# Optimization experiments

Hardware: AMD Instinct MI355X
Metric: run time of the kernel (lower is better)

## Reference

```python
import jax, jax.numpy as jnp
import numpy as np

B, N, D, H = 8, 4096, 256, 4
KP, KN = N // 16, N // 32
EPS = 1e-6

def _ln(x, g, b):
    m = jnp.mean(x, -1, keepdims=True)
    v = jnp.var(x, -1, keepdims=True)
    return (x - m) / jnp.sqrt(v + 1e-5) * g + b

def _cross_attn(q_in, kv_in, wq, wk, wv, wo, bo):
    # q_in [1,Nq,D], kv_in [1,Nk,D]
    Bq, Nq, Dm = q_in.shape
    Nk = kv_in.shape[1]
    dh = Dm // H
    q = (q_in @ wq).reshape(Bq, Nq, H, dh).transpose(0, 2, 1, 3)
    k = (kv_in @ wk).reshape(Bq, Nk, H, dh).transpose(0, 2, 1, 3)
    v = (kv_in @ wv).reshape(Bq, Nk, H, dh).transpose(0, 2, 1, 3)
    attn = jax.nn.softmax(jnp.einsum('bhqd,bhkd->bhqk', q, k) * (dh ** -0.5), axis=-1)
    out = jnp.einsum('bhqk,bhkd->bhqd', attn, v).transpose(0, 2, 1, 3).reshape(Bq, Nq, Dm)
    return out @ wo + bo

def setup_inputs():
    key = jax.random.key(0)
    ks = jax.random.split(key, 40)
    f32 = jnp.float32
    def w(i, shape, s):
        return s * jax.random.normal(ks[i], shape, f32)
    inp = {}
    inp['x'] = jax.random.normal(ks[0], (B, N, D), f32)
    inp['mask'] = (jax.random.randint(ks[1], (B, N), 0, 3) - 1).astype(jnp.int32)  # values in {-1,0,1}
    inp['pos_emb'] = 0.02 * jax.random.normal(ks[2], (1, N, D), f32)
    inp['sim_p_w'] = w(3, (D, D), 0.2); inp['sim_p_b'] = jnp.zeros((D,), f32)
    inp['sim_n_w'] = w(4, (D, D), 0.2); inp['sim_n_b'] = jnp.zeros((D,), f32)
    inp['adj_w'] = w(5, (D, D), 0.05)
    inp['gnn_p_w1'] = w(6, (D, D), 0.05); inp['gnn_p_w2'] = w(7, (D, D), 0.05)
    inp['gnn_n_w1'] = w(8, (D, D), 0.05); inp['gnn_n_w2'] = w(9, (D, D), 0.05)
    for i in range(1, 6):
        inp['ln%d_g' % i] = jnp.ones((D,), f32)
        inp['ln%d_b' % i] = jnp.zeros((D,), f32)
    names = ['i2q_wq', 'i2q_wk', 'i2q_wv', 'i2q_wo', 'q2i_wq', 'q2i_wk', 'q2i_wv', 'q2i_wo']
    for j, nme in enumerate(names):
        inp[nme] = w(10 + j, (D, D), 0.05)
    inp['i2q_bo'] = jnp.zeros((D,), f32)
    inp['q2i_bo'] = jnp.zeros((D,), f32)
    inp['mlp_w'] = w(20, (D, D), 0.05); inp['mlp_b'] = jnp.zeros((D,), f32)
    inp['g_i2t'] = 0.1 * jax.random.normal(ks[21], (1, 1, D), f32)
    inp['g_t2i'] = 0.1 * jax.random.normal(ks[22], (1, 1, D), f32)
    return inp

def reference(x, mask, pos_emb, sim_p_w, sim_p_b, sim_n_w, sim_n_b, adj_w,
              gnn_p_w1, gnn_p_w2, gnn_n_w1, gnn_n_w2,
              ln1_g, ln1_b, ln2_g, ln2_b, ln3_g, ln3_b, ln4_g, ln4_b, ln5_g, ln5_b,
              i2q_wq, i2q_wk, i2q_wv, i2q_wo, i2q_bo,
              q2i_wq, q2i_wk, q2i_wv, q2i_wo, q2i_bo,
              mlp_w, mlp_b, g_i2t, g_t2i):
    pos_mask = (mask == 1).astype(x.dtype)[..., None]    # [B,N,1]
    neg_mask = (mask == -1).astype(x.dtype)[..., None]
    pos_query = (x * pos_mask).sum(1, keepdims=True) / (pos_mask.sum(1, keepdims=True) + EPS)  # [B,1,D]
    neg_query = (x * neg_mask).sum(1, keepdims=True) / (neg_mask.sum(1, keepdims=True) + EPS)
    pos_sim = jax.nn.sigmoid(((x @ sim_p_w + sim_p_b) * pos_query).sum(-1))  # [B,N]
    neg_sim = jax.nn.sigmoid(((x @ sim_n_w + sim_n_b) * neg_query).sum(-1))
    weight_p, idx_p = jax.lax.top_k(pos_sim, KP)
    weight_n, idx_n = jax.lax.top_k(neg_sim, KN)
    scale = 1.0 / jnp.sqrt(jnp.asarray(D, x.dtype))

    def gcn(node, w1, w2):
        adj = jax.nn.softmax((node @ adj_w) @ node.T * scale, axis=-1)  # [K,K]
        h = jax.nn.relu(adj @ (node @ w1))
        return adj @ (h @ w2)

    def batch_forward(ip, wp, inn, wn, feat):
        node_p = feat[ip] * (wp > 0.6).astype(feat.dtype)[:, None]       # [KP,D]
        query_p = gcn(node_p, gnn_p_w1, gnn_p_w2) + pos_emb[0, ip]
        node_n = feat[inn] * (wn > 0.6).astype(feat.dtype)[:, None]      # [KN,D]
        query_n = gcn(node_n, gnn_n_w1, gnn_n_w2) + pos_emb[0, inn]
        query = jnp.concatenate([query_p, query_n], 0)[None]             # [1,KP+KN,D]
        featb = feat[None]                                               # [1,N,D]
        query = query + g_i2t * _cross_attn(_ln(query, ln1_g, ln1_b), _ln(featb, ln2_g, ln2_b),
                                            i2q_wq, i2q_wk, i2q_wv, i2q_wo, i2q_bo)
        featb = featb + g_t2i * _cross_attn(_ln(featb, ln3_g, ln3_b), _ln(query, ln4_g, ln4_b),
                                            q2i_wq, q2i_wk, q2i_wv, q2i_wo, q2i_bo)
        featb = featb + (_ln(featb, ln5_g, ln5_b) @ mlp_w + mlp_b)
        return featb

    out = jax.vmap(batch_forward)(idx_p, weight_p, idx_n, weight_n, x)   # [B,1,N,D]
    return out, pos_sim, neg_sim
```

## Files before the change

### kernel.cpp

```cpp
#include <hip/hip_runtime.h>

#define BB 8
#define NN 4096
#define DD 256
#define HH 4
#define DHH 64
#define KPP 256
#define KNN 128
#define SCH 64

typedef float f32x4 __attribute__((ext_vector_type(4)));
typedef short bf16x8 __attribute__((ext_vector_type(8)));
typedef short bf16x4 __attribute__((ext_vector_type(4)));

#define FLAG_TRANSB 1
#define FLAG_RELU   2

__device__ __forceinline__ float bf2f(unsigned short u){
  union { unsigned int i; float f; } v; v.i = ((unsigned int)u) << 16; return v.f;
}
__device__ __forceinline__ unsigned short f2bf(float f){
  union { float f; unsigned int i; } v; v.f = f;
  return (unsigned short)((v.i + 0x7FFFu + ((v.i >> 16) & 1u)) >> 16);
}
__device__ __forceinline__ void gload16(const void* g, void* l){
  __builtin_amdgcn_global_load_lds((const __attribute__((address_space(1))) void*)g,
                                   (__attribute__((address_space(3))) void*)l, 16, 0, 0);
}

__global__ __launch_bounds__(256) void stats_part(const float* __restrict__ x,
                                                  const int* __restrict__ mask,
                                                  float* __restrict__ part,
                                                  float* __restrict__ pcnt){
  int b = blockIdx.y, c = blockIdx.x, t = threadIdx.x;
  int w = t >> 6, lane = t & 63;
  const int R = NN / SCH;
  int n0 = c * R;
  const float* xb = x + ((long)b*NN + n0)*DD;
  const int* mb = mask + (long)b*NN + n0;
// ... 71 lines not shown
  float s  = xv.x+xv.y+xv.z+xv.w;
  float q  = xv.x*xv.x+xv.y*xv.y+xv.z*xv.z+xv.w*xv.w;
  for (int off = 32; off; off >>= 1){
    sp += __shfl_xor(sp, off); sn += __shfl_xor(sn, off);
    s  += __shfl_xor(s, off);  q  += __shfl_xor(q, off);
  }
  float m = s*(1.f/256.f);
  float var = q*(1.f/256.f) - m*m;
  float rinv = rsqrtf(var + 1e-5f);
  ushort4 o;
  o.x = f2bf((xv.x-m)*rinv); o.y = f2bf((xv.y-m)*rinv);
  o.z = f2bf((xv.z-m)*rinv); o.w = f2bf((xv.w-m)*rinv);
  ((ushort4*)(xhat + row*DD))[lane] = o;
  if (lane == 0){
    float zp = sp + cscal[b*2+0], zn = sn + cscal[b*2+1];
    simP[row] = 1.f/(1.f+expf(-zp));
    simN[row] = 1.f/(1.f+expf(-zn));
  }
}

__global__ __launch_bounds__(256) void topk_radix(const float* __restrict__ simP,
                                                  const float* __restrict__ simN,
                                                  const float* __restrict__ x,
                                                  int* __restrict__ idxb, float* __restrict__ wb,
                                                  float* __restrict__ node){
  __shared__ unsigned int vals[4096];
  __shared__ unsigned int hist[4096];
  __shared__ unsigned short eql[4096];
  __shared__ unsigned int tsum[256];
  __shared__ unsigned int sB, sRem, sCG, sCnt, sEq;
  int id = blockIdx.x; int sgn = id & 1, b = id >> 1;
  int K = (sgn == 0) ? KPP : KNN;
  const float* s = (sgn == 0 ? simP : simN) + (long)b*NN;
  int t = threadIdx.x;
  if (t == 0){ sCG = 0; sCnt = 0; sEq = 0; }
  for (int i = t; i < 4096; i += 256){ vals[i] = __float_as_uint(s[i]); hist[i] = 0; }
  __syncthreads();

  auto find_thresh = [&](int NB, unsigned need){
    int per = NB >> 8;
    int base = t*per;
    unsigned local = 0;
    for (int j = 0; j < per; j++) local += hist[base+j];
    tsum[t] = local;
    __syncthreads();
    #pragma unroll
    for (int st = 1; st < 256; st <<= 1){
      unsigned v = (t + st < 256) ? tsum[t+st] : 0u;
// ... 29 lines not shown
    unsigned v = vals[i];
    if ((v >> 20) == B1) atomicAdd(&hist[(v >> 8) & 0xFFFu], 1u);
  }
  __syncthreads();
  find_thresh(4096, rem1);
  unsigned B2 = sB, rem2 = sRem;
  unsigned pre = (B1 << 12) | B2;
  __syncthreads();
  hist[t] = 0;
  __syncthreads();
  for (int i = t; i < 4096; i += 256){
    unsigned v = vals[i];
    if ((v >> 8) == pre) atomicAdd(&hist[v & 0xFFu], 1u);
  }
  __syncthreads();
  find_thresh(256, rem2);
  unsigned T = (pre << 8) | sB;
  unsigned cg = sCG;
  __syncthreads();
  hist[t] = 0;
  __syncthreads();

  int* oi = idxb + (long)id*256;
  float* ow = wb + (long)id*256;
  for (int i = t; i < 4096; i += 256){
    unsigned v = vals[i];
    if (v > T){
      unsigned p = atomicAdd(&sCnt, 1u);
      oi[p] = i; ow[p] = __uint_as_float(v);
      hist[p] = (unsigned)i; hist[256+p] = v;
    }
    else if (v == T){ unsigned e = atomicAdd(&sEq, 1u); eql[e] = (unsigned short)i; }
  }
  __syncthreads();
  int ne = K - (int)cg;
  int eqn = (int)sEq;
  for (int e = t; e < eqn; e += 256){
    int myi = eql[e]; int r = 0;
    for (int e2 = 0; e2 < eqn; e2++) r += (eql[e2] < myi);
    if (r < ne){
      oi[cg + r] = myi; ow[cg + r] = __uint_as_float(T);
      hist[cg + r] = (unsigned)myi; hist[256 + cg + r] = T;
    }
  }
  __syncthreads();
  int rbase = (sgn == 0) ? 0 : KPP;
  int lane = t & 63, rw = t >> 6;
  for (int i0 = 0; i0 < K; i0 += 4){
    int r = i0 + rw;
    int idx = (int)hist[r];
    float wv = __uint_as_float(hist[256 + r]);
    float4 vsel;
    if (wv > 0.6f) vsel = ((const float4*)(x + ((long)b*NN + idx)*DD))[lane];
    else vsel = (float4){0.f,0.f,0.f,0.f};
    ((float4*)(node + ((long)b*384 + rbase + r)*DD))[lane] = vsel;
  }
}

__global__ void softmax_dual(float* __restrict__ A0, int L0, int rpb0, long bs0, int rows0,
                             float* __restrict__ A1, int L1, int rpb1, long bs1, int rows1){
  int w = threadIdx.x >> 6, lane = threadIdx.x & 63;
  long row = (long)blockIdx.x*4 + w;
  float* A; int L, rpb; long bs;
  if (row < rows0){ A = A0; L = L0; rpb = rpb0; bs = bs0; }
  else { row -= rows0; if (row >= rows1) return; A = A1; L = L1; rpb = rpb1; bs = bs1; }
  int b = (int)(row / rpb), r = (int)(row % rpb);
  float* a = A + (long)b*bs + (long)r*L;
  int e = L >> 6;
  float vals[4]; float mx = -1e30f;
  for (int j = 0; j < e; j++){ vals[j] = a[lane*e+j]; mx = fmaxf(mx, vals[j]); }
  for (int off = 32; off; off >>= 1) mx = fmaxf(mx, __shfl_xor(mx, off));
  float sum = 0.f;
  for (int j = 0; j < e; j++){ vals[j] = expf(vals[j]-mx); sum += vals[j]; }
  for (int off = 32; off; off >>= 1) sum += __shfl_xor(sum, off);
  float rinv = 1.f/sum;
  for (int j = 0; j < e; j++) a[lane*e+j] = vals[j]*rinv;
}

__global__ void rownorm_kernel(const float* __restrict__ X, unsigned short* __restrict__ Y, int rows){
  int w = threadIdx.x >> 6, lane = threadIdx.x & 63;
  long row = (long)blockIdx.x*4 + w;
  if (row >= rows) return;
  const float4* xr = (const float4*)(X + row*DD);
  float4 xv = xr[lane];
  float s = xv.x+xv.y+xv.z+xv.w;
  float q = xv.x*xv.x+xv.y*xv.y+xv.z*xv.z+xv.w*xv.w;
  for (int off = 32; off; off >>= 1){ s += __shfl_xor(s, off); q += __shfl_xor(q, off); }
  float m = s*(1.f/256.f);
  float var = q*(1.f/256.f) - m*m;
  float rinv = rsqrtf(var + 1e-5f);
  ushort4 o;
  o.x = f2bf((xv.x-m)*rinv); o.y = f2bf((xv.y-m)*rinv);
  o.z = f2bf((xv.z-m)*rinv); o.w = f2bf((xv.w-m)*rinv);
  ((ushort4*)(Y + row*DD))[lane] = o;
}

struct FoldArgs { const float* W[9]; const float* g[9]; unsigned short* BT[9]; };
struct BiasArgs { const float* W[7]; const float* b[7]; const float* addb[7]; float* out[7]; };

__global__ void fold_w(FoldArgs fa){
  int m = blockIdx.y, tile = blockIdx.x, t = threadIdx.x;
  const float* W = fa.W[m]; const float* g = fa.g[m]; unsigned short* BT = fa.BT[m];
  __shared__ float T[64][65];
  int tn = (tile & 3)*64, tk = (tile >> 2)*64;
  #pragma unroll 4
  for (int p = 0; p < 16; p++){
    int kl = p*4 + (t >> 6), nl = t & 63;
    float v = W[(long)(tk+kl)*256 + tn + nl];
    if (g) v *= g[tk+kl];
    T[kl][nl] = v;
  }
  __syncthreads();
  #pragma unroll 4
  for (int p = 0; p < 16; p++){
    int nl = p*4 + (t >> 6), kl = t & 63;
    BT[(long)(tn+nl)*256 + tk + kl] = f2bf(T[kl][nl]);
  }
}

__global__ void fold_b(BiasArgs ba){
  int m = blockIdx.x, n = threadIdx.x;
  const float* W = ba.W[m]; const float* b = ba.b[m];
  float s = (ba.addb[m] != nullptr) ? ba.addb[m][n] : 0.f;
  for (int k = 0; k < 256; k++) s += b[k]*W[(long)k*256+n];
  ba.out[m][n] = s;
}

struct GP {
  const float* A; long sAb; int lda;
  const float* B; long sBb; int ldb;
  float* C; long sCb; int ldc;
  const int* pidx; const float* pe;
  int M, N, K; float alpha; int flags;
};
struct GP4 { GP p[4]; };

__global__ __launch_bounds__(256) void gemm_multi(GP4 g4){
  GP p = g4.p[blockIdx.z >> 3];
  int b = blockIdx.z & 7;
  int m0 = blockIdx.y*64, n0 = blockIdx.x*64;
  if (m0 >= p.M || n0 >= p.N) return;
  __shared__ __align__(16) unsigned short As[64*40];
  __shared__ __align__(16) unsigned short Bs[64*40];
  const float* Ab = p.A + (long)b*p.sAb;
  const float* Bb = p.B + (long)b*p.sBb;
  int t = threadIdx.x;
  int w = t >> 6, lane = t & 63, lrowi = lane & 15, lquad = lane >> 4;
  int wm = w >> 1, wn = w & 1;
  f32x4 acc[2][2];
  #pragma unroll
  for (int i = 0; i < 2; i++)
    #pragma unroll
    for (int j = 0; j < 2; j++) acc[i][j] = (f32x4){0.f,0.f,0.f,0.f};
  int am = t >> 2, akq = t & 3;
  for (int k0 = 0; k0 < p.K; k0 += 32){
    {
      const float4* s4 = (const float4*)(Ab + (long)(m0+am)*p.lda + k0 + akq*8);
      float4 u = s4[0], vv = s4[1];
      unsigned short tmp[8];
      tmp[0]=f2bf(u.x); tmp[1]=f2bf(u.y); tmp[2]=f2bf(u.z); tmp[3]=f2bf(u.w);
      tmp[4]=f2bf(vv.x); tmp[5]=f2bf(vv.y); tmp[6]=f2bf(vv.z); tmp[7]=f2bf(vv.w);
      *(uint4*)(&As[am*40 + akq*8]) = *(uint4*)tmp;
    }
    if (p.flags & FLAG_TRANSB){
      const float4* s4 = (const float4*)(Bb + (long)(n0+am)*p.ldb + k0 + akq*8);
      float4 u = s4[0], vv = s4[1];
      unsigned short tmp[8];
      tmp[0]=f2bf(u.x); tmp[1]=f2bf(u.y); tmp[2]=f2bf(u.z); tmp[3]=f2bf(u.w);
      tmp[4]=f2bf(vv.x); tmp[5]=f2bf(vv.y); tmp[6]=f2bf(vv.z); tmp[7]=f2bf(vv.w);
      *(uint4*)(&Bs[am*40 + akq*8]) = *(uint4*)tmp;
    } else {
      int bn = t & 63, bkb = (t >> 6)*8;
      #pragma unroll
      for (int j = 0; j < 8; j++)
        Bs[bn*40 + bkb + j] = f2bf(Bb[(long)(k0+bkb+j)*p.ldb + n0 + bn]);
    }
    __syncthreads();
    bf16x8 af[2], bfr[2];
    #pragma unroll
    for (int i = 0; i < 2; i++)
      af[i] = *(const bf16x8*)(&As[(wm*32 + i*16 + lrowi)*40 + lquad*8]);
    #pragma unroll
    for (int j = 0; j < 2; j++)
      bfr[j] = *(const bf16x8*)(&Bs[(wn*32 + j*16 + lrowi)*40 + lquad*8]);
    #pragma unroll
    for (int i = 0; i < 2; i++)
      #pragma unroll
      for (int j = 0; j < 2; j++)
        acc[i][j] = __builtin_amdgcn_mfma_f32_16x16x32_bf16(af[i], bfr[j], acc[i][j], 0, 0, 0);
    __syncthreads();
  }
  float* Cb = p.C + (long)b*p.sCb;
  #pragma unroll
  for (int i = 0; i < 2; i++)
    #pragma unroll
    for (int j = 0; j < 2; j++){
      int col = n0 + wn*32 + j*16 + lrowi;
      #pragma unroll
      for (int r = 0; r < 4; r++){
        int row = m0 + wm*32 + i*16 + lquad*4 + r;
        float v = p.alpha*acc[i][j][r];
        if (p.flags & FLAG_RELU) v = fmaxf(v, 0.f);
        if (p.pidx != nullptr){
          int idx = p.pidx[b*512 + row];
          v += p.pe[(long)idx*256 + col];
        }
        Cb[(long)row*p.ldc + col] = v;
      }
    }
}

template<typename OT, bool RES, bool GATE>
__global__ __launch_bounds__(256) void gemm128(
    const unsigned short* __restrict__ A, long sAb,
    const unsigned short* __restrict__ BT,
    OT* __restrict__ C, long sCb, int ldc,
    const float* __restrict__ R, long sRb,
    const float* __restrict__ bias, const float* __restrict__ gate)
{
  __shared__ __align__(16) unsigned short As[4096];
  __shared__ __align__(16) unsigned short Bs[4096];
  int t = threadIdx.x;
  int w = t >> 6, lane = t & 63, lrowi = lane & 15, lquad = lane >> 4;
  int wm = w >> 1, wn = w & 1;
  int m0 = blockIdx.y*128, n0 = blockIdx.x*128;
  const unsigned short* Ab = A + (long)blockIdx.z*sAb + (long)m0*256;
  const unsigned short* Bb = BT + (long)n0*256;
  int g0 = t, g1 = 256 + t;
  int row0 = g0 >> 2, kq0 = g0 & 3;
  int row1 = g1 >> 2, kq1 = g1 & 3;
  f32x4 acc[4][4];
  #pragma unroll
// ... 32 lines not shown
    for (int i = 0; i < 4; i++){
      #pragma unroll
      for (int r = 0; r < 4; r++){
        int row = m0 + wm*64 + i*16 + lquad*4 + r;
        float v = acc[i][j][r] + bv;
        if (GATE) v *= gv;
        if (RES) v += Rb[(long)row*256 + col];
        if constexpr (sizeof(OT) == 4) Cb[(long)row*ldc + col] = v;
        else                           Cb[(long)row*ldc + col] = f2bf(v);
      }
    }
  }
}

template<int NFRAG>
__global__ __launch_bounds__(256) void flash_kernel(
    const unsigned short* __restrict__ Q, long sQb, int ldq,
    const unsigned short* __restrict__ Kt, const unsigned short* __restrict__ Vt,
    long sKb, int ldkv,
    unsigned short* __restrict__ O, long sOb,
    float* __restrict__ Opart, float* __restrict__ Lpart,
    int Nq, int Nk, int nsplit, float scale)
{
  __shared__ __align__(16) unsigned short Kl[32*72];
  __shared__ __align__(16) unsigned short Vl[64*36];
  __shared__ __align__(16) unsigned short Pl[4*NFRAG*16*36];
  int b = blockIdx.z, h = blockIdx.y;
  int nqg = Nq / (64*NFRAG);
  int qg = blockIdx.x % nqg, split = blockIdx.x / nqg;
  int kchunk = Nk / nsplit;
  int kbeg = split*kchunk, kend = kbeg + kchunk;
  int t = threadIdx.x, w = t >> 6, lane = t & 63, lrowi = lane & 15, lquad = lane >> 4;
  int q0 = qg*(64*NFRAG) + w*(16*NFRAG);
  const unsigned short* Qb = Q + (long)b*sQb + h*DHH;
  const unsigned short* Kb = Kt + (long)b*sKb + h*DHH;
  const unsigned short* Vb = Vt + (long)b*sKb + h*DHH;
  bf16x8 qa[NFRAG][2];
  #pragma unroll
  for (int f = 0; f < NFRAG; f++)
    #pragma unroll
    for (int kt = 0; kt < 2; kt++)
      qa[f][kt] = *(const bf16x8*)(Qb + (long)(q0 + f*16 + lrowi)*ldq + kt*32 + lquad*8);

  f32x4 o[NFRAG][4];
  float psum[NFRAG][4];
  #pragma unroll
  for (int f = 0; f < NFRAG; f++)
    #pragma unroll
    for (int cj = 0; cj < 4; cj++){
      o[f][cj] = (f32x4){0.f,0.f,0.f,0.f};
      psum[f][cj] = 0.f;
    }
  int skq = t >> 3, sdq = (t & 7)*8;
  int vkq = t & 31, vdq = (t >> 5)*8;
  unsigned short* Pw = &Pl[w*(NFRAG*16*36)];
  const float ec = scale * 1.44269504089f;

  for (int kt0 = kbeg; kt0 < kend; kt0 += 32){
    {
      uint4 kv = *(const uint4*)(Kb + (long)(kt0+skq)*ldkv + sdq);
      *(uint4*)(&Kl[skq*72 + sdq]) = kv;
      uint4 vv = *(const uint4*)(Vb + (long)(kt0+vkq)*ldkv + vdq);
      const unsigned short* vp = (const unsigned short*)&vv;
      #pragma unroll
      for (int j = 0; j < 8; j++) Vl[(vdq+j)*36 + vkq] = vp[j];
    }
    __syncthreads();
    bf16x8 kb0 = *(const bf16x8*)(&Kl[(0*16+lrowi)*72 + lquad*8]);
    bf16x8 kb1 = *(const bf16x8*)(&Kl[(0*16+lrowi)*72 + 32 + lquad*8]);
    bf16x8 kb2 = *(const bf16x8*)(&Kl[(1*16+lrowi)*72 + lquad*8]);
    bf16x8 kb3 = *(const bf16x8*)(&Kl[(1*16+lrowi)*72 + 32 + lquad*8]);
    union { bf16x8 v8; bf16x4 v4[2]; } vbu[4];
    #pragma unroll
    for (int cj = 0; cj < 4; cj++){
      const unsigned short* vb = &Vl[(cj*16+lrowi)*36 + lquad*8];
      vbu[cj].v4[0] = *(const bf16x4*)vb;
      vbu[cj].v4[1] = *(const bf16x4*)(vb + 4);
    }
    #pragma unroll
    for (int f = 0; f < NFRAG; f++){
      f32x4 S0 = (f32x4){0.f,0.f,0.f,0.f}, S1 = (f32x4){0.f,0.f,0.f,0.f};
      S0 = __builtin_amdgcn_mfma_f32_16x16x32_bf16(qa[f][0], kb0, S0, 0, 0, 0);
      S0 = __builtin_amdgcn_mfma_f32_16x16x32_bf16(qa[f][1], kb1, S0, 0, 0, 0);
      S1 = __builtin_amdgcn_mfma_f32_16x16x32_bf16(qa[f][0], kb2, S1, 0, 0, 0);
      S1 = __builtin_amdgcn_mfma_f32_16x16x32_bf16(qa[f][1], kb3, S1, 0, 0, 0);
      unsigned short* Pf = Pw + f*(16*36);
      #pragma unroll
      for (int r = 0; r < 4; r++){
        float p0 = exp2f(S0[r]*ec);
        float p1 = exp2f(S1[r]*ec);
        psum[f][r] += p0 + p1;
        Pf[(lquad*4+r)*36 + lrowi]      = f2bf(p0);
        Pf[(lquad*4+r)*36 + 16 + lrowi] = f2bf(p1);
      }
    }
    __asm__ volatile("s_waitcnt lgkmcnt(0)" ::: "memory");
    #pragma unroll
    for (int f = 0; f < NFRAG; f++){
      const unsigned short* pp = &Pw[f*(16*36) + lrowi*36 + lquad*8];
      union { bf16x8 v8; bf16x4 v4[2]; } pa;
      pa.v4[0] = *(const bf16x4*)pp;
      pa.v4[1] = *(const bf16x4*)(pp + 4);
      #pragma unroll
      for (int cj = 0; cj < 4; cj++)
        o[f][cj] = __builtin_amdgcn_mfma_f32_16x16x32_bf16(pa.v8, vbu[cj].v8, o[f][cj], 0, 0, 0);
    }
    __syncthreads();
  }
  float lsum[NFRAG][4];
  #pragma unroll
  for (int f = 0; f < NFRAG; f++)
    #pragma unroll
    for (int r = 0; r < 4; r++){
      float s = psum[f][r];
      #pragma unroll
      for (int off = 1; off < 16; off <<= 1) s += __shfl_xor(s, off);
      lsum[f][r] = s;
    }
  if (nsplit > 1){
    int p = (b*HH + h)*nsplit + split;
    float* Op = Opart + (long)p*Nq*DHH;
    #pragma unroll
    for (int f = 0; f < NFRAG; f++)
      #pragma unroll
      for (int r = 0; r < 4; r++){
        int row = q0 + f*16 + lquad*4 + r;
        #pragma unroll
        for (int cj = 0; cj < 4; cj++)
// ... 62 lines not shown
  const float* i2q_bo = (const float*)d_in[30];
  const float* q2i_bo = (const float*)d_in[31];
  const float* mlp_w  = (const float*)d_in[32];
  const float* mlp_b  = (const float*)d_in[33];
  const float* g_i2t  = (const float*)d_in[34];
  const float* g_t2i  = (const float*)d_in[35];

  float* out  = (float*)d_out;
  float* simP = out + (size_t)BB*NN*DD;
  float* simN = simP + (size_t)BB*NN;

  char* w8 = (char*)d_ws;
  size_t off = 0;
  auto take = [&](size_t bytes)->void*{
    void* p = (void*)(w8 + off);
    off += (bytes + 255) & ~(size_t)255;
    return p;
  };
  float* part   = (float*)take((size_t)BB*SCH*2*DD*4);
  float* pcnt   = (float*)take((size_t)BB*SCH*2*4);
  float* vvec   = (float*)take((size_t)BB*2*DD*4);
  float* cscal  = (float*)take((size_t)BB*2*4);
  int*   idxb   = (int*)take((size_t)BB*2*256*4);
  float* wb     = (float*)take((size_t)BB*2*256*4);
  float* node   = (float*)take((size_t)BB*384*DD*4);
  float* gA     = (float*)take((size_t)BB*384*DD*4);
  float* gadjP  = (float*)take((size_t)BB*256*256*4);
  float* gadjN  = (float*)take((size_t)BB*128*128*4);
  float* query  = (float*)take((size_t)BB*384*DD*4);
  float* query2 = (float*)take((size_t)BB*384*DD*4);
  unsigned short* xhatq  = (unsigned short*)take((size_t)BB*384*DD*2);
  unsigned short* qh     = (unsigned short*)take((size_t)BB*384*DD*2);
  unsigned short* attnZ  = (unsigned short*)take((size_t)BB*384*DD*2);
  unsigned short* xhatq2 = (unsigned short*)take((size_t)BB*384*DD*2);
  unsigned short* kv2    = (unsigned short*)take((size_t)BB*384*512*2);
  unsigned short* xhat   = (unsigned short*)take((size_t)BB*NN*DD*2);
  unsigned short* kvq    = (unsigned short*)take((size_t)BB*NN*768*2);
  float* featb2 = (float*)take((size_t)BB*NN*DD*4);
  float* Lpart  = (float*)take((size_t)BB*HH*8*384*4);
  unsigned short* wTq1  = (unsigned short*)take((size_t)65536*2);
  unsigned short* wTbig = (unsigned short*)take((size_t)3*65536*2);
  unsigned short* wTkv2 = (unsigned short*)take((size_t)2*65536*2);
  unsigned short* wTmlp = (unsigned short*)take((size_t)65536*2);
  unsigned short* wTo1  = (unsigned short*)take((size_t)65536*2);
  unsigned short* wTo2  = (unsigned short*)take((size_t)65536*2);
  float* biasQ1  = (float*)take(256*4);
  float* biasBig = (float*)take(768*4);
  float* biasKV2 = (float*)take(512*4);
  float* biasMlp = (float*)take(256*4);
  float* t1 = query;
  float* t2 = query2;
  float* t3 = gA;
  unsigned short* attn2 = xhat;
  unsigned short* xhat5 = kvq;
  float* Opart = featb2;

  const long sQ  = 384L*DD;
  const long sX  = (long)NN*DD;
  const float* NF = nullptr;

  FoldArgs fa;
  fa.W[0]=i2q_wq; fa.g[0]=ln1_g; fa.BT[0]=wTq1;
  fa.W[1]=i2q_wk; fa.g[1]=ln2_g; fa.BT[1]=wTbig;
  fa.W[2]=i2q_wv; fa.g[2]=ln2_g; fa.BT[2]=wTbig + 256*256;
  fa.W[3]=q2i_wq; fa.g[3]=ln3_g; fa.BT[3]=wTbig + 512*256;
  fa.W[4]=q2i_wk; fa.g[4]=ln4_g; fa.BT[4]=wTkv2;
  fa.W[5]=q2i_wv; fa.g[5]=ln4_g; fa.BT[5]=wTkv2 + 256*256;
  fa.W[6]=mlp_w;  fa.g[6]=ln5_g; fa.BT[6]=wTmlp;
  fa.W[7]=i2q_wo; fa.g[7]=nullptr; fa.BT[7]=wTo1;
  fa.W[8]=q2i_wo; fa.g[8]=nullptr; fa.BT[8]=wTo2;
  fold_w<<<dim3(16,9), 256, 0, stream>>>(fa);
  BiasArgs ba;
  ba.W[0]=i2q_wq; ba.b[0]=ln1_b; ba.addb[0]=nullptr; ba.out[0]=biasQ1;
  ba.W[1]=i2q_wk; ba.b[1]=ln2_b; ba.addb[1]=nullptr; ba.out[1]=biasBig;
  ba.W[2]=i2q_wv; ba.b[2]=ln2_b; ba.addb[2]=nullptr; ba.out[2]=biasBig+256;
  ba.W[3]=q2i_wq; ba.b[3]=ln3_b; ba.addb[3]=nullptr; ba.out[3]=biasBig+512;
  ba.W[4]=q2i_wk; ba.b[4]=ln4_b; ba.addb[4]=nullptr; ba.out[4]=biasKV2;
  ba.W[5]=q2i_wv; ba.b[5]=ln4_b; ba.addb[5]=nullptr; ba.out[5]=biasKV2+256;
  ba.W[6]=mlp_w;  ba.b[6]=ln5_b; ba.addb[6]=mlp_b;   ba.out[6]=biasMlp;
  fold_b<<<7, 256, 0, stream>>>(ba);

  stats_part<<<dim3(SCH, BB), 256, 0, stream>>>(x, mask, part, pcnt);
  stats_vec<<<BB, 256, 0, stream>>>(part, pcnt, sim_p_w, sim_p_b, sim_n_w, sim_n_b, vvec, cscal);
  sim_norm_kernel<<<dim3(NN/4, BB), 256, 0, stream>>>(x, vvec, cscal, simP, simN, xhat);
  topk_radix<<<2*BB, 256, 0, stream>>>(simP, simN, x, idxb, wb, node);

  GP z = {};
  {
    GP4 g;
    g.p[0] = { node, 384L*DD, 256, adj_w, 0, 256, gA, 384L*DD, 256, nullptr, nullptr, 384, 256, 256, 1.f, 0 };
    g.p[1] = { node, 384L*DD, 256, gnn_p_w1, 0, 256, t1, 384L*DD, 256, nullptr, nullptr, 256, 256, 256, 1.f, 0 };
    g.p[2] = { node + 256L*DD, 384L*DD, 256, gnn_n_w1, 0, 256, t1 + 256L*DD, 384L*DD, 256, nullptr, nullptr, 128, 256, 256, 1.f, 0 };
    g.p[3] = z;
    gemm_multi<<<dim3(4,6,3*BB), 256, 0, stream>>>(g);
  }
  {
    GP4 g;
    g.p[0] = { gA, 384L*DD, 256, node, 384L*DD, 256, gadjP, 65536L, 256, nullptr, nullptr, 256, 256, 256, 0.0625f, FLAG_TRANSB };
    g.p[1] = { gA + 256L*DD, 384L*DD, 256, node + 256L*DD, 384L*DD, 256, gadjN, 16384L, 128, nullptr, nullptr, 128, 128, 256, 0.0625f, FLAG_TRANSB };
    g.p[2] = z; g.p[3] = z;
    gemm_multi<<<dim3(4,4,2*BB), 256, 0, stream>>>(g);
  }
  softmax_dual<<<768, 256, 0, stream>>>(gadjP, 256, 256, 65536L, BB*256,
                                        gadjN, 128, 128, 16384L, BB*128);
  {
    GP4 g;
    g.p[0] = { gadjP, 65536L, 256, t1, 384L*DD, 256, t2, 384L*DD, 256, nullptr, nullptr, 256, 256, 256, 1.f, FLAG_RELU };
    g.p[1] = { gadjN, 16384L, 128, t1 + 256L*DD, 384L*DD, 256, t2 + 256L*DD, 384L*DD, 256, nullptr, nullptr, 128, 256, 128, 1.f, FLAG_RELU };
    g.p[2] = z; g.p[3] = z;
    gemm_multi<<<dim3(4,4,2*BB), 256, 0, stream>>>(g);
  }
  {
    GP4 g;
    g.p[0] = { t2, 384L*DD, 256, gnn_p_w2, 0, 256, t3, 384L*DD, 256, nullptr, nullptr, 256, 256, 256, 1.f, 0 };
    g.p[1] = { t2 + 256L*DD, 384L*DD, 256, gnn_n_w2, 0, 256, t3 + 256L*DD, 384L*DD, 256, nullptr, nullptr, 128, 256, 256, 1.f, 0 };
    g.p[2] = z; g.p[3] = z;
    gemm_multi<<<dim3(4,4,2*BB), 256, 0, stream>>>(g);
  }
  {
    GP4 g;
    g.p[0] = { gadjP, 65536L, 256, t3, 384L*DD, 256, query, 384L*DD, 256, idxb, pos_emb, 256, 256, 256, 1.f, 0 };
    g.p[1] = { gadjN, 16384L, 128, t3 + 256L*DD, 384L*DD, 256, query + 256L*DD, 384L*DD, 256, idxb + 256, pos_emb, 128, 256, 128, 1.f, 0 };
    g.p[2] = z; g.p[3] = z;
    gemm_multi<<<dim3(4,4,2*BB), 256, 0, stream>>>(g);
  }

  rownorm_kernel<<<BB*384/4, 256, 0, stream>>>(query, xhatq, BB*384);

  gemm128<unsigned short,false,false><<<dim3(2,3,BB),256,0,stream>>>(
      xhatq, sQ, wTq1, qh, sQ, 256, NF, 0, biasQ1, NF);
  gemm128<unsigned short,false,false><<<dim3(6,32,BB),256,0,stream>>>(
      xhat, sX, wTbig, kvq, (long)NN*768, 768, NF, 0, biasBig, NF);
  flash_kernel<3><<<dim3(2*8, HH, BB), 256, 0, stream>>>(
      qh, sQ, 256, kvq, kvq + 256, (long)NN*768, 768,
      attnZ, sQ, Opart, Lpart, 384, NN, 8, 0.125f);
  flash_combine<<<BB*HH*384/4, 256, 0, stream>>>(Opart, Lpart, attnZ, sQ, 384, 8);
  gemm128<float,true,true><<<dim3(2,3,BB),256,0,stream>>>(
      attnZ, sQ, wTo1, query2, sQ, 256, query, sQ, i2q_bo, g_i2t);

  rownorm_kernel<<<BB*384/4, 256, 0, stream>>>(query2, xhatq2, BB*384);
  gemm128<unsigned short,false,false><<<dim3(4,3,BB),256,0,stream>>>(
      xhatq2, sQ, wTkv2, kv2, 384L*512, 512, NF, 0, biasKV2, NF);
  flash_kernel<2><<<dim3(32, HH, BB), 256, 0, stream>>>(
      kvq + 512, (long)NN*768, 768, kv2, kv2 + 256, 384L*512, 512,
      attn2, sX, nullptr, nullptr, NN, 384, 1, 0.125f);
  gemm128<float,true,true><<<dim3(2,32,BB),256,0,stream>>>(
      attn2, sX, wTo2, featb2, sX, 256, x, sX, q2i_bo, g_t2i);
// ... 6 lines not shown
```

Baseline: 498.6 us.

## Convert GCN chain to bf16 NT GEMMs with async LDS loads; widen flash K tile

The GCN stage now keeps node features, adjacency, and intermediate products in bf16. Weights are pre-transposed in fold_w, and each product is arranged so both operands are K-contiguous. This lets a new 128x128 GEMM load tiles straight into LDS with global_load_lds instead of converting fp32 on the fly, and it removes the strided transpose-B path. Separately, the flash attention inner loop now processes 64 keys per iteration with packed V transposes and truncating bf16 conversion of P. The cost is extra bf16 buffers, more rounding in intermediate GCN results, and larger LDS and register use per block.

```diff
diff --git a/kernel.cpp b/kernel.cpp
--- a/kernel.cpp
+++ b/kernel.cpp
@@ -11,10 +11,9 @@
 
 typedef float f32x4 __attribute__((ext_vector_type(4)));
 typedef short bf16x8 __attribute__((ext_vector_type(8)));
-typedef short bf16x4 __attribute__((ext_vector_type(4)));
-
-#define FLAG_TRANSB 1
-#define FLAG_RELU   2
+
+#define FLAG_RELU   1
+#define FLAG_OUTF32 2
 
 __device__ __forceinline__ float bf2f(unsigned short u){
   union { unsigned int i; float f; } v; v.i = ((unsigned int)u) << 16; return v.f;
@@ -132,8 +131,8 @@
 __global__ __launch_bounds__(256) void topk_radix(const float* __restrict__ simP,
                                                   const float* __restrict__ simN,
                                                   const float* __restrict__ x,
-                                                  int* __restrict__ idxb, float* __restrict__ wb,
-                                                  float* __restrict__ node){
+                                                  int* __restrict__ idxb,
+                                                  unsigned short* __restrict__ node_bf){
   __shared__ unsigned int vals[4096];
   __shared__ unsigned int hist[4096];
   __shared__ unsigned short eql[4096];
@@ -209,12 +208,11 @@
   __syncthreads();
 
   int* oi = idxb + (long)id*256;
-  float* ow = wb + (long)id*256;
   for (int i = t; i < 4096; i += 256){
     unsigned v = vals[i];
     if (v > T){
       unsigned p = atomicAdd(&sCnt, 1u);
-      oi[p] = i; ow[p] = __uint_as_float(v);
+      oi[p] = i;
       hist[p] = (unsigned)i; hist[256+p] = v;
     }
     else if (v == T){ unsigned e = atomicAdd(&sEq, 1u); eql[e] = (unsigned short)i; }
@@ -226,7 +224,7 @@
     int myi = eql[e]; int r = 0;
     for (int e2 = 0; e2 < eqn; e2++) r += (eql[e2] < myi);
     if (r < ne){
-      oi[cg + r] = myi; ow[cg + r] = __uint_as_float(T);
+      oi[cg + r] = myi;
       hist[cg + r] = (unsigned)myi; hist[256 + cg + r] = T;
     }
   }
@@ -240,19 +238,24 @@
     float4 vsel;
     if (wv > 0.6f) vsel = ((const float4*)(x + ((long)b*NN + idx)*DD))[lane];
     else vsel = (float4){0.f,0.f,0.f,0.f};
-    ((float4*)(node + ((long)b*384 + rbase + r)*DD))[lane] = vsel;
-  }
-}
-
-__global__ void softmax_dual(float* __restrict__ A0, int L0, int rpb0, long bs0, int rows0,
-                             float* __restrict__ A1, int L1, int rpb1, long bs1, int rows1){
+    ushort4 ov;
+    ov.x = f2bf(vsel.x); ov.y = f2bf(vsel.y); ov.z = f2bf(vsel.z); ov.w = f2bf(vsel.w);
+    ((ushort4*)(node_bf + ((long)b*384 + rbase + r)*DD))[lane] = ov;
+  }
+}
+
+__global__ void softmax_dual(const float* __restrict__ A0, unsigned short* __restrict__ O0,
+                             int L0, int rpb0, long bs0, int rows0,
+                             const float* __restrict__ A1, unsigned short* __restrict__ O1,
+                             int L1, int rpb1, long bs1, int rows1){
   int w = threadIdx.x >> 6, lane = threadIdx.x & 63;
   long row = (long)blockIdx.x*4 + w;
-  float* A; int L, rpb; long bs;
-  if (row < rows0){ A = A0; L = L0; rpb = rpb0; bs = bs0; }
-  else { row -= rows0; if (row >= rows1) return; A = A1; L = L1; rpb = rpb1; bs = bs1; }
+  const float* A; unsigned short* O; int L, rpb; long bs;
+  if (row < rows0){ A = A0; O = O0; L = L0; rpb = rpb0; bs = bs0; }
+  else { row -= rows0; if (row >= rows1) return; A = A1; O = O1; L = L1; rpb = rpb1; bs = bs1; }
   int b = (int)(row / rpb), r = (int)(row % rpb);
-  float* a = A + (long)b*bs + (long)r*L;
+  const float* a = A + (long)b*bs + (long)r*L;
+  unsigned short* o = O + (long)b*bs + (long)r*L;
   int e = L >> 6;
   float vals[4]; float mx = -1e30f;
   for (int j = 0; j < e; j++){ vals[j] = a[lane*e+j]; mx = fmaxf(mx, vals[j]); }
@@ -261,7 +264,7 @@
   for (int j = 0; j < e; j++){ vals[j] = expf(vals[j]-mx); sum += vals[j]; }
   for (int off = 32; off; off >>= 1) sum += __shfl_xor(sum, off);
   float rinv = 1.f/sum;
-  for (int j = 0; j < e; j++) a[lane*e+j] = vals[j]*rinv;
+  for (int j = 0; j < e; j++) o[lane*e+j] = f2bf(vals[j]*rinv);
 }
 
 __global__ void rownorm_kernel(const float* __restrict__ X, unsigned short* __restrict__ Y, int rows){
@@ -282,7 +285,7 @@
   ((ushort4*)(Y + row*DD))[lane] = o;
 }
 
-struct FoldArgs { const float* W[9]; const float* g[9]; unsigned short* BT[9]; };
+struct FoldArgs { const float* W[14]; const float* g[14]; unsigned short* BT[14]; };
 struct BiasArgs { const float* W[7]; const float* b[7]; const float* addb[7]; float* out[7]; };
 
 __global__ void fold_w(FoldArgs fa){
@@ -313,88 +316,78 @@
   ba.out[m][n] = s;
 }
 
-struct GP {
-  const float* A; long sAb; int lda;
-  const float* B; long sBb; int ldb;
-  float* C; long sCb; int ldc;
+struct GX {
+  const unsigned short* A; long sAb; int lda;
+  const unsigned short* B; long sBb; int ldb;
+  void* C; long sCb; int ldc;
   const int* pidx; const float* pe;
   int M, N, K; float alpha; int flags;
 };
-struct GP4 { GP p[4]; };
-
-__global__ __launch_bounds__(256) void gemm_multi(GP4 g4){
-  GP p = g4.p[blockIdx.z >> 3];
+struct GX4 { GX p[4]; };
+
+__global__ __launch_bounds__(256) void gemmx(GX4 g4){
+  GX p = g4.p[blockIdx.z >> 3];
   int b = blockIdx.z & 7;
-  int m0 = blockIdx.y*64, n0 = blockIdx.x*64;
+  int m0 = blockIdx.y*128, n0 = blockIdx.x*128;
   if (m0 >= p.M || n0 >= p.N) return;
-  __shared__ __align__(16) unsigned short As[64*40];
-  __shared__ __align__(16) unsigned short Bs[64*40];
-  const float* Ab = p.A + (long)b*p.sAb;
-  const float* Bb = p.B + (long)b*p.sBb;
+  __shared__ __align__(16) unsigned short As[4096];
+  __shared__ __align__(16) unsigned short Bs[4096];
   int t = threadIdx.x;
   int w = t >> 6, lane = t & 63, lrowi = lane & 15, lquad = lane >> 4;
   int wm = w >> 1, wn = w & 1;
-  f32x4 acc[2][2];
+  const unsigned short* Ab = p.A + (long)b*p.sAb + (long)m0*p.lda;
+  const unsigned short* Bb = p.B + (long)b*p.sBb + (long)n0*p.ldb;
+  int g0 = t, g1 = 256 + t;
+  int row0 = g0 >> 2, kq0 = g0 & 3;
+  int row1 = g1 >> 2, kq1 = g1 & 3;
+  f32x4 acc[4][4];
   #pragma unroll
-  for (int i = 0; i < 2; i++)
-    #pragma unroll
-    for (int j = 0; j < 2; j++) acc[i][j] = (f32x4){0.f,0.f,0.f,0.f};
-  int am = t >> 2, akq = t & 3;
+  for (int i = 0; i < 4; i++)
+    #pragma unroll
+    for (int j = 0; j < 4; j++) acc[i][j] = (f32x4){0.f,0.f,0.f,0.f};
+
   for (int k0 = 0; k0 < p.K; k0 += 32){
-    {
-      const float4* s4 = (const float4*)(Ab + (long)(m0+am)*p.lda + k0 + akq*8);
-      float4 u = s4[0], vv = s4[1];
-      unsigned short tmp[8];
-      tmp[0]=f2bf(u.x); tmp[1]=f2bf(u.y); tmp[2]=f2bf(u.z); tmp[3]=f2bf(u.w);
-      tmp[4]=f2bf(vv.x); tmp[5]=f2bf(vv.y); tmp[6]=f2bf(vv.z); tmp[7]=f2bf(vv.w);
-      *(uint4*)(&As[am*40 + akq*8]) = *(uint4*)tmp;
-    }
-    if (p.flags & FLAG_TRANSB){
-      const float4* s4 = (const float4*)(Bb + (long)(n0+am)*p.ldb + k0 + akq*8);
-      float4 u = s4[0], vv = s4[1];
-      unsigned short tmp[8];
-      tmp[0]=f2bf(u.x); tmp[1]=f2bf(u.y); tmp[2]=f2bf(u.z); tmp[3]=f2bf(u.w);
-      tmp[4]=f2bf(vv.x); tmp[5]=f2bf(vv.y); tmp[6]=f2bf(vv.z); tmp[7]=f2bf(vv.w);
-      *(uint4*)(&Bs[am*40 + akq*8]) = *(uint4*)tmp;
-    } else {
-      int bn = t & 63, bkb = (t >> 6)*8;
-      #pragma unroll
-      for (int j = 0; j < 8; j++)
-        Bs[bn*40 + bkb + j] = f2bf(Bb[(long)(k0+bkb+j)*p.ldb + n0 + bn]);
-    }
+    gload16(Ab + (long)row0*p.lda + k0 + kq0*8, &As[g0*8]);
+    gload16(Ab + (long)row1*p.lda + k0 + kq1*8, &As[g1*8]);
+    gload16(Bb + (long)row0*p.ldb + k0 + kq0*8, &Bs[g0*8]);
+    gload16(Bb + (long)row1*p.ldb + k0 + kq1*8, &Bs[g1*8]);
     __syncthreads();
-    bf16x8 af[2], bfr[2];
-    #pragma unroll
-    for (int i = 0; i < 2; i++)
-      af[i] = *(const bf16x8*)(&As[(wm*32 + i*16 + lrowi)*40 + lquad*8]);
-    #pragma unroll
-    for (int j = 0; j < 2; j++)
-      bfr[j] = *(const bf16x8*)(&Bs[(wn*32 + j*16 + lrowi)*40 + lquad*8]);
-    #pragma unroll
-    for (int i = 0; i < 2; i++)
-      #pragma unroll
-      for (int j = 0; j < 2; j++)
+    bf16x8 af[4], bfr[4];
+    #pragma unroll
+    for (int i = 0; i < 4; i++)
+      af[i] = *(const bf16x8*)(&As[((wm*64 + i*16 + lrowi)*4 + lquad)*8]);
+    #pragma unroll
+    for (int j = 0; j < 4; j++)
+      bfr[j] = *(const bf16x8*)(&Bs[((wn*64 + j*16 + lrowi)*4 + lquad)*8]);
+    #pragma unroll
+    for (int i = 0; i < 4; i++)
+      #pragma unroll
+      for (int j = 0; j < 4; j++)
         acc[i][j] = __builtin_amdgcn_mfma_f32_16x16x32_bf16(af[i], bfr[j], acc[i][j], 0, 0, 0);
     __syncthreads();
   }
-  float* Cb = p.C + (long)b*p.sCb;
+  char* Cb = (char*)p.C;
   #pragma unroll
-  for (int i = 0; i < 2; i++)
-    #pragma unroll
-    for (int j = 0; j < 2; j++){
-      int col = n0 + wn*32 + j*16 + lrowi;
+  for (int j = 0; j < 4; j++){
+    int col = n0 + wn*64 + j*16 + lrowi;
+    #pragma unroll
+    for (int i = 0; i < 4; i++){
       #pragma unroll
       for (int r = 0; r < 4; r++){
-        int row = m0 + wm*32 + i*16 + lquad*4 + r;
+        int row = m0 + wm*64 + i*16 + lquad*4 + r;
         float v = p.alpha*acc[i][j][r];
         if (p.flags & FLAG_RELU) v = fmaxf(v, 0.f);
         if (p.pidx != nullptr){
           int idx = p.pidx[b*512 + row];
           v += p.pe[(long)idx*256 + col];
         }
-        Cb[(long)row*p.ldc + col] = v;
+        if (p.flags & FLAG_OUTF32)
+          ((float*)Cb)[b*p.sCb + (long)row*p.ldc + col] = v;
+        else
+          ((unsigned short*)Cb)[b*p.sCb + (long)row*p.ldc + col] = f2bf(v);
       }
     }
+  }
 }
 
 template<typename OT, bool RES, bool GATE>
@@ -473,9 +466,9 @@
     float* __restrict__ Opart, float* __restrict__ Lpart,
     int Nq, int Nk, int nsplit, float scale)
 {
-  __shared__ __align__(16) unsigned short Kl[32*72];
-  __shared__ __align__(16) unsigned short Vl[64*36];
-  __shared__ __align__(16) unsigned short Pl[4*NFRAG*16*36];
+  __shared__ __align__(16) unsigned short Kl[64*72];
+  __shared__ __align__(16) unsigned short Vl[64*72];
+  __shared__ __align__(16) unsigned short Pl[4*NFRAG*16*72];
   int b = blockIdx.z, h = blockIdx.y;
   int nqg = Nq / (64*NFRAG);
   int qg = blockIdx.x % nqg, split = blockIdx.x / nqg;
@@ -503,58 +496,68 @@
       psum[f][cj] = 0.f;
     }
   int skq = t >> 3, sdq = (t & 7)*8;
-  int vkq = t & 31, vdq = (t >> 5)*8;
-  unsigned short* Pw = &Pl[w*(NFRAG*16*36)];
+  int vkp = t & 31, vdg = t >> 5;
+  unsigned short* Pw = &Pl[w*(NFRAG*16*72)];
   const float ec = scale * 1.44269504089f;
 
-  for (int kt0 = kbeg; kt0 < kend; kt0 += 32){
+  for (int kt0 = kbeg; kt0 < kend; kt0 += 64){
     {
-      uint4 kv = *(const uint4*)(Kb + (long)(kt0+skq)*ldkv + sdq);
-      *(uint4*)(&Kl[skq*72 + sdq]) = kv;
-      uint4 vv = *(const uint4*)(Vb + (long)(kt0+vkq)*ldkv + vdq);
-      const unsigned short* vp = (const unsigned short*)&vv;
-      #pragma unroll
-      for (int j = 0; j < 8; j++) Vl[(vdq+j)*36 + vkq] = vp[j];
+      uint4 k0v = *(const uint4*)(Kb + (long)(kt0+skq)*ldkv + sdq);
+      *(uint4*)(&Kl[skq*72 + sdq]) = k0v;
+      uint4 k1v = *(const uint4*)(Kb + (long)(kt0+32+skq)*ldkv + sdq);
+      *(uint4*)(&Kl[(32+skq)*72 + sdq]) = k1v;
+      uint4 v0 = *(const uint4*)(Vb + (long)(kt0+2*vkp)*ldkv + vdg*8);
+      uint4 v1 = *(const uint4*)(Vb + (long)(kt0+2*vkp+1)*ldkv + vdg*8);
+      const unsigned short* p0 = (const unsigned short*)&v0;
+      const unsigned short* p1 = (const unsigned short*)&v1;
+      #pragma unroll
+      for (int j = 0; j < 8; j++){
+        unsigned pk = (unsigned)p0[j] | ((unsigned)p1[j] << 16);
+        *(unsigned*)(&Vl[(vdg*8+j)*72 + 2*vkp]) = pk;
+      }
     }
     __syncthreads();
-    bf16x8 kb0 = *(const bf16x8*)(&Kl[(0*16+lrowi)*72 + lquad*8]);
-    bf16x8 kb1 = *(const bf16x8*)(&Kl[(0*16+lrowi)*72 + 32 + lquad*8]);
-    bf16x8 kb2 = *(const bf16x8*)(&Kl[(1*16+lrowi)*72 + lquad*8]);
-    bf16x8 kb3 = *(const bf16x8*)(&Kl[(1*16+lrowi)*72 + 32 + lquad*8]);
-    union { bf16x8 v8; bf16x4 v4[2]; } vbu[4];
+    bf16x8 kbf[4][2];
+    #pragma unroll
+    for (int ct = 0; ct < 4; ct++){
+      kbf[ct][0] = *(const bf16x8*)(&Kl[(ct*16+lrowi)*72 + lquad*8]);
+      kbf[ct][1] = *(const bf16x8*)(&Kl[(ct*16+lrowi)*72 + 32 + lquad*8]);
+    }
+    #pragma unroll
+    for (int f = 0; f < NFRAG; f++){
+      f32x4 S[4];
+      #pragma unroll
+      for (int ct = 0; ct < 4; ct++){
+        S[ct] = (f32x4){0.f,0.f,0.f,0.f};
+        S[ct] = __builtin_amdgcn_mfma_f32_16x16x32_bf16(qa[f][0], kbf[ct][0], S[ct], 0, 0, 0);
+        S[ct] = __builtin_amdgcn_mfma_f32_16x16x32_bf16(qa[f][1], kbf[ct][1], S[ct], 0, 0, 0);
+      }
+      unsigned short* Pf = Pw + f*(16*72);
+      #pragma unroll
+      for (int ct = 0; ct < 4; ct++)
+        #pragma unroll
+        for (int r = 0; r < 4; r++){
+          float p = exp2f(S[ct][r]*ec);
+          psum[f][r] += p;
+          Pf[(lquad*4+r)*72 + ct*16 + lrowi] = (unsigned short)(__float_as_uint(p) >> 16);
+        }
+    }
+    __asm__ volatile("s_waitcnt lgkmcnt(0)" ::: "memory");
+    bf16x8 vbf[4][2];
     #pragma unroll
     for (int cj = 0; cj < 4; cj++){
-      const unsigned short* vb = &Vl[(cj*16+lrowi)*36 + lquad*8];
-      vbu[cj].v4[0] = *(const bf16x4*)vb;
-      vbu[cj].v4[1] = *(const bf16x4*)(vb + 4);
+      vbf[cj][0] = *(const bf16x8*)(&Vl[(cj*16+lrowi)*72 + lquad*8]);
+      vbf[cj][1] = *(const bf16x8*)(&Vl[(cj*16+lrowi)*72 + 32 + lquad*8]);
     }
     #pragma unroll
     for (int f = 0; f < NFRAG; f++){
-      f32x4 S0 = (f32x4){0.f,0.f,0.f,0.f}, S1 = (f32x4){0.f,0.f,0.f,0.f};
-      S0 = __builtin_amdgcn_mfma_f32_16x16x32_bf16(qa[f][0], kb0, S0, 0, 0, 0);
-      S0 = __builtin_amdgcn_mfma_f32_16x16x32_bf16(qa[f][1], kb1, S0, 0, 0, 0);
-      S1 = __builtin_amdgcn_mfma_f32_16x16x32_bf16(qa[f][0], kb2, S1, 0, 0, 0);
-      S1 = __builtin_amdgcn_mfma_f32_16x16x32_bf16(qa[f][1], kb3, S1, 0, 0, 0);
-      unsigned short* Pf = Pw + f*(16*36);
-      #pragma unroll
-      for (int r = 0; r < 4; r++){
-        float p0 = exp2f(S0[r]*ec);
-        float p1 = exp2f(S1[r]*ec);
-        psum[f][r] += p0 + p1;
-        Pf[(lquad*4+r)*36 + lrowi]      = f2bf(p0);
-        Pf[(lquad*4+r)*36 + 16 + lrowi] = f2bf(p1);
+      bf16x8 pa0 = *(const bf16x8*)(&Pw[f*(16*72) + lrowi*72 + lquad*8]);
+      bf16x8 pa1 = *(const bf16x8*)(&Pw[f*(16*72) + lrowi*72 + 32 + lquad*8]);
+      #pragma unroll
+      for (int cj = 0; cj < 4; cj++){
+        o[f][cj] = __builtin_amdgcn_mfma_f32_16x16x32_bf16(pa0, vbf[cj][0], o[f][cj], 0, 0, 0);
+        o[f][cj] = __builtin_amdgcn_mfma_f32_16x16x32_bf16(pa1, vbf[cj][1], o[f][cj], 0, 0, 0);
       }
-    }
-    __asm__ volatile("s_waitcnt lgkmcnt(0)" ::: "memory");
-    #pragma unroll
-    for (int f = 0; f < NFRAG; f++){
-      const unsigned short* pp = &Pw[f*(16*36) + lrowi*36 + lquad*8];
-      union { bf16x8 v8; bf16x4 v4[2]; } pa;
-      pa.v4[0] = *(const bf16x4*)pp;
-      pa.v4[1] = *(const bf16x4*)(pp + 4);
-      #pragma unroll
-      for (int cj = 0; cj < 4; cj++)
-        o[f][cj] = __builtin_amdgcn_mfma_f32_16x16x32_bf16(pa.v8, vbu[cj].v8, o[f][cj], 0, 0, 0);
     }
     __syncthreads();
   }
@@ -663,9 +666,16 @@
   float* vvec   = (float*)take((size_t)BB*2*DD*4);
   float* cscal  = (float*)take((size_t)BB*2*4);
   int*   idxb   = (int*)take((size_t)BB*2*256*4);
-  float* wb     = (float*)take((size_t)BB*2*256*4);
-  float* node   = (float*)take((size_t)BB*384*DD*4);
-  float* gA     = (float*)take((size_t)BB*384*DD*4);
+  unsigned short* node_bf = (unsigned short*)take((size_t)BB*384*DD*2);
+  unsigned short* gAb   = (unsigned short*)take((size_t)BB*384*DD*2);
+  unsigned short* t1Tp  = (unsigned short*)take((size_t)BB*256*256*2);
+  unsigned short* t1Tn  = (unsigned short*)take((size_t)BB*256*128*2);
+  unsigned short* t2p   = (unsigned short*)take((size_t)BB*256*256*2);
+  unsigned short* t2n   = (unsigned short*)take((size_t)BB*128*256*2);
+  unsigned short* t3Tp  = (unsigned short*)take((size_t)BB*256*256*2);
+  unsigned short* t3Tn  = (unsigned short*)take((size_t)BB*256*128*2);
+  unsigned short* adjPb = (unsigned short*)take((size_t)BB*256*256*2);
+  unsigned short* adjNb = (unsigned short*)take((size_t)BB*128*128*2);
   float* gadjP  = (float*)take((size_t)BB*256*256*4);
   float* gadjN  = (float*)take((size_t)BB*128*128*4);
   float* query  = (float*)take((size_t)BB*384*DD*4);
@@ -685,13 +695,15 @@
   unsigned short* wTmlp = (unsigned short*)take((size_t)65536*2);
   unsigned short* wTo1  = (unsigned short*)take((size_t)65536*2);
   unsigned short* wTo2  = (unsigned short*)take((size_t)65536*2);
+  unsigned short* wTadj = (unsigned short*)take((size_t)65536*2);
+  unsigned short* wTp1  = (unsigned short*)take((size_t)65536*2);
+  unsigned short* wTp2  = (unsigned short*)take((size_t)65536*2);
+  unsigned short* wTn1  = (unsigned short*)take((size_t)65536*2);
+  unsigned short* wTn2  = (unsigned short*)take((size_t)65536*2);
   float* biasQ1  = (float*)take(256*4);
   float* biasBig = (float*)take(768*4);
   float* biasKV2 = (float*)take(512*4);
   float* biasMlp = (float*)take(256*4);
-  float* t1 = query;
-  float* t2 = query2;
-  float* t3 = gA;
   unsigned short* attn2 = xhat;
   unsigned short* xhat5 = kvq;
   float* Opart = featb2;
@@ -710,7 +722,12 @@
   fa.W[6]=mlp_w;  fa.g[6]=ln5_g; fa.BT[6]=wTmlp;
   fa.W[7]=i2q_wo; fa.g[7]=nullptr; fa.BT[7]=wTo1;
   fa.W[8]=q2i_wo; fa.g[8]=nullptr; fa.BT[8]=wTo2;
-  fold_w<<<dim3(16,9), 256, 0, stream>>>(fa);
+  fa.W[9]=adj_w;    fa.g[9]=nullptr;  fa.BT[9]=wTadj;
+  fa.W[10]=gnn_p_w1; fa.g[10]=nullptr; fa.BT[10]=wTp1;
+  fa.W[11]=gnn_p_w2; fa.g[11]=nullptr; fa.BT[11]=wTp2;
+  fa.W[12]=gnn_n_w1; fa.g[12]=nullptr; fa.BT[12]=wTn1;
+  fa.W[13]=gnn_n_w2; fa.g[13]=nullptr; fa.BT[13]=wTn2;
+  fold_w<<<dim3(16,14), 256, 0, stream>>>(fa);
   BiasArgs ba;
   ba.W[0]=i2q_wq; ba.b[0]=ln1_b; ba.addb[0]=nullptr; ba.out[0]=biasQ1;
   ba.W[1]=i2q_wk; ba.b[1]=ln2_b; ba.addb[1]=nullptr; ba.out[1]=biasBig;
@@ -724,46 +741,47 @@
   stats_part<<<dim3(SCH, BB), 256, 0, stream>>>(x, mask, part, pcnt);
   stats_vec<<<BB, 256, 0, stream>>>(part, pcnt, sim_p_w, sim_p_b, sim_n_w, sim_n_b, vvec, cscal);
   sim_norm_kernel<<<dim3(NN/4, BB), 256, 0, stream>>>(x, vvec, cscal, simP, simN, xhat);
-  topk_radix<<<2*BB, 256, 0, stream>>>(simP, simN, x, idxb, wb, node);
-
-  GP z = {};
+  topk_radix<<<2*BB, 256, 0, stream>>>(simP, simN, x, idxb, node_bf);
+
+  GX z = {};
+  const long sN = 384L*256;
   {
-    GP4 g;
-    g.p[0] = { node, 384L*DD, 256, adj_w, 0, 256, gA, 384L*DD, 256, nullptr, nullptr, 384, 256, 256, 1.f, 0 };
-    g.p[1] = { node, 384L*DD, 256, gnn_p_w1, 0, 256, t1, 384L*DD, 256, nullptr, nullptr, 256, 256, 256, 1.f, 0 };
-    g.p[2] = { node + 256L*DD, 384L*DD, 256, gnn_n_w1, 0, 256, t1 + 256L*DD, 384L*DD, 256, nullptr, nullptr, 128, 256, 256, 1.f, 0 };
+    GX4 g;
+    g.p[0] = { node_bf, sN, 256, wTadj, 0, 256, gAb, sN, 256, nullptr, nullptr, 384, 256, 256, 1.f, 0 };
+    g.p[1] = { wTp1, 0, 256, node_bf, sN, 256, t1Tp, 256L*256, 256, nullptr, nullptr, 256, 256, 256, 1.f, 0 };
+    g.p[2] = { wTn1, 0, 256, node_bf + 256*256, sN, 256, t1Tn, 256L*128, 128, nullptr, nullptr, 256, 128, 256, 1.f, 0 };
     g.p[3] = z;
-    gemm_multi<<<dim3(4,6,3*BB), 256, 0, stream>>>(g);
+    gemmx<<<dim3(2,3,24), 256, 0, stream>>>(g);
   }
   {
-    GP4 g;
-    g.p[0] = { gA, 384L*DD, 256, node, 384L*DD, 256, gadjP, 65536L, 256, nullptr, nullptr, 256, 256, 256, 0.0625f, FLAG_TRANSB };
-    g.p[1] = { gA + 256L*DD, 384L*DD, 256, node + 256L*DD, 384L*DD, 256, gadjN, 16384L, 128, nullptr, nullptr, 128, 128, 256, 0.0625f, FLAG_TRANSB };
+    GX4 g;
+    g.p[0] = { gAb, sN, 256, node_bf, sN, 256, gadjP, 65536L, 256, nullptr, nullptr, 256, 256, 256, 0.0625f, FLAG_OUTF32 };
+    g.p[1] = { gAb + 256*256, sN, 256, node_bf + 256*256, sN, 256, gadjN, 16384L, 128, nullptr, nullptr, 128, 128, 256, 0.0625f, FLAG_OUTF32 };
     g.p[2] = z; g.p[3] = z;
-    gemm_multi<<<dim3(4,4,2*BB), 256, 0, stream>>>(g);
-  }
-  softmax_dual<<<768, 256, 0, stream>>>(gadjP, 256, 256, 65536L, BB*256,
-                                        gadjN, 128, 128, 16384L, BB*128);
+    gemmx<<<dim3(2,2,16), 256, 0, stream>>>(g);
+  }
+  softmax_dual<<<768, 256, 0, stream>>>(gadjP, adjPb, 256, 256, 65536L, BB*256,
+                                        gadjN, adjNb, 128, 128, 16384L, BB*128);
   {
-    GP4 g;
-    g.p[0] = { gadjP, 65536L, 256, t1, 384L*DD, 256, t2, 384L*DD, 256, nullptr, nullptr, 256, 256, 256, 1.f, FLAG_RELU };
-    g.p[1] = { gadjN, 16384L, 128, t1 + 256L*DD, 384L*DD, 256, t2 + 256L*DD, 384L*DD, 256, nullptr, nullptr, 128, 256, 128, 1.f, FLAG_RELU };
+    GX4 g;
+    g.p[0] = { adjPb, 65536L, 256, t1Tp, 256L*256, 256, t2p, 256L*256, 256, nullptr, nullptr, 256, 256, 256, 1.f, FLAG_RELU };
+    g.p[1] = { adjNb, 16384L, 128, t1Tn, 256L*128, 128, t2n, 128L*256, 256, nullptr, nullptr, 128, 256, 128, 1.f, FLAG_RELU };
     g.p[2] = z; g.p[3] = z;
-    gemm_multi<<<dim3(4,4,2*BB), 256, 0, stream>>>(g);
+    gemmx<<<dim3(2,2,16), 256, 0, stream>>>(g);
   }
   {
-    GP4 g;
-    g.p[0] = { t2, 384L*DD, 256, gnn_p_w2, 0, 256, t3, 384L*DD, 256, nullptr, nullptr, 256, 256, 256, 1.f, 0 };
-    g.p[1] = { t2 + 256L*DD, 384L*DD, 256, gnn_n_w2, 0, 256, t3 + 256L*DD, 384L*DD, 256, nullptr, nullptr, 128, 256, 256, 1.f, 0 };
+    GX4 g;
+    g.p[0] = { wTp2, 0, 256, t2p, 256L*256, 256, t3Tp, 256L*256, 256, nullptr, nullptr, 256, 256, 256, 1.f, 0 };
+    g.p[1] = { wTn2, 0, 256, t2n, 128L*256, 256, t3Tn, 256L*128, 128, nullptr, nullptr, 256, 128, 256, 1.f, 0 };
     g.p[2] = z; g.p[3] = z;
-    gemm_multi<<<dim3(4,4,2*BB), 256, 0, stream>>>(g);
+    gemmx<<<dim3(2,2,16), 256, 0, stream>>>(g);
   }
   {
-    GP4 g;
-    g.p[0] = { gadjP, 65536L, 256, t3, 384L*DD, 256, query, 384L*DD, 256, idxb, pos_emb, 256, 256, 256, 1.f, 0 };
-    g.p[1] = { gadjN, 16384L, 128, t3 + 256L*DD, 384L*DD, 256, query + 256L*DD, 384L*DD, 256, idxb + 256, pos_emb, 128, 256, 128, 1.f, 0 };
+    GX4 g;
+    g.p[0] = { adjPb, 65536L, 256, t3Tp, 256L*256, 256, query, sQ, 256, idxb, pos_emb, 256, 256, 256, 1.f, FLAG_OUTF32 };
+    g.p[1] = { adjNb, 16384L, 128, t3Tn, 256L*128, 128, query + 256*256, sQ, 256, idxb + 256, pos_emb, 128, 256, 128, 1.f, FLAG_OUTF32 };
     g.p[2] = z; g.p[3] = z;
-    gemm_multi<<<dim3(4,4,2*BB), 256, 0, stream>>>(g);
+    gemmx<<<dim3(2,2,16), 256, 0, stream>>>(g);
   }
 
   rownorm_kernel<<<BB*384/4, 256, 0, stream>>>(query, xhatq, BB*384);
```

Result: slower. 516.0 us (+3.5%).
